# Optimization experiments

Hardware: AMD Instinct MI355X
Metric: run time of the kernel (lower is better)

Reference implementation:

```python
import jax, jax.numpy as jnp
import numpy as np

N, E, IN, HID, HEADS, OUT = 50000, 800000, 128, 64, 4, 64


def setup_inputs() -> dict:
    key = jax.random.key(0)
    ks = jax.random.split(key, 13)
    s1 = 1.0 / np.sqrt(IN)
    s2 = 1.0 / np.sqrt(HID * HEADS)
    s3 = 1.0 / np.sqrt(HID)
    return {
        'x': jax.random.normal(ks[0], (N, IN), dtype=jnp.float32),
        'edge_index': jax.random.randint(ks[1], (2, E), 0, N, dtype=jnp.int64),
        # GATv2 layer 1: heads=HEADS, out=HID, concat=True
        'W1l': jax.random.normal(ks[2], (IN, HEADS * HID), dtype=jnp.float32) * s1,
        'W1r': jax.random.normal(ks[3], (IN, HEADS * HID), dtype=jnp.float32) * s1,
        'att1': jax.random.normal(ks[4], (HEADS, HID), dtype=jnp.float32) * s3,
        'b1': jnp.zeros((HEADS * HID,), dtype=jnp.float32),
        # GATv2 layer 2: heads=1, out=HID
        'W2l': jax.random.normal(ks[5], (HEADS * HID, HID), dtype=jnp.float32) * s2,
        'W2r': jax.random.normal(ks[6], (HEADS * HID, HID), dtype=jnp.float32) * s2,
        'att2': jax.random.normal(ks[7], (1, HID), dtype=jnp.float32) * s3,
        'b2': jnp.zeros((HID,), dtype=jnp.float32),
        # final Linear(HID, OUT)
        'Wlin': jax.random.normal(ks[8], (HID, OUT), dtype=jnp.float32) * s3,
        'blin': jnp.zeros((OUT,), dtype=jnp.float32),
    }


def _gatv2(x, src, dst, Wl, Wr, att, bias, n):
    # PyG GATv2Conv (share_weights=False): x_j -> lin_l, x_i -> lin_r
    H, C = att.shape
    xl = (x @ Wl).reshape(n, H, C)  # source transform [N,H,C]
    xr = (x @ Wr).reshape(n, H, C)  # destination transform [N,H,C]
    # per-edge GATv2 score: a^T LeakyReLU(xl_j + xr_i)
    e = jnp.sum(jax.nn.leaky_relu(xl[src] + xr[dst], 0.2) * att, axis=-1)  # [E,H]
    # scatter-softmax over edges sharing a destination
    m = jax.ops.segment_max(e, dst, num_segments=n)  # [N,H]
    ex = jnp.exp(e - m[dst])
    denom = jax.ops.segment_sum(ex, dst, num_segments=n)
    alpha = ex / (denom[dst] + 1e-16)  # [E,H]
    # weighted scatter-add aggregation of source features
    out = jax.ops.segment_sum(xl[src] * alpha[:, :, None], dst, num_segments=n)  # [N,H,C]
    return out.reshape(n, H * C) + bias


def reference(x, edge_index, W1l, W1r, att1, b1, W2l, W2r, att2, b2, Wlin, blin):
    n = x.shape[0]
    loops = jnp.arange(n, dtype=edge_index.dtype)
    src = jnp.concatenate([edge_index[0], loops])  # add_self_loops=True (PyG default)
    dst = jnp.concatenate([edge_index[1], loops])
    h = _gatv2(x, src, dst, W1l, W1r, att1, b1, n)
    h = jax.nn.elu(h)
    h = _gatv2(h, src, dst, W2l, W2r, att2, b2, n)
    h = jax.nn.elu(h)
    return h @ Wlin + blin
```

## Files before the change

### kernel.cpp

```cpp
#include <hip/hip_runtime.h>
#include <hip/hip_bf16.h>
#include <math.h>

#define N_NODES 50000
#define N_EDGES 800000
#define ETOT (N_EDGES + N_NODES)
#define NB_SCAN 196

typedef __attribute__((ext_vector_type(8))) short short8;
typedef __attribute__((ext_vector_type(4))) float floatx4;
typedef __attribute__((ext_vector_type(2))) float f32x2;

__device__ __forceinline__ float bf_lo(unsigned u) { return __uint_as_float(u << 16); }
__device__ __forceinline__ float bf_hi(unsigned u) { return __uint_as_float(u & 0xffff0000u); }
__device__ __forceinline__ unsigned short f2bf(float f) {
    unsigned u = __float_as_uint(f);
    return (unsigned short)((u + 0x7fffu + ((u >> 16) & 1u)) >> 16);
}
__device__ __forceinline__ unsigned pack2bf(float a, float b) {
    return (unsigned)f2bf(a) | ((unsigned)f2bf(b) << 16);
}
#define DPP_ADD(p, ctrl) \
    (p) += __int_as_float(__builtin_amdgcn_update_dpp(0, __float_as_int(p), (ctrl), 0xF, 0xF, true))

__global__ __launch_bounds__(256) void k_prep(const float* __restrict__ W1l,
                                              const float* __restrict__ W1r,
                                              const float* __restrict__ W2l,
                                              const float* __restrict__ W2r,
                                              const float* __restrict__ Wlin,
                                              unsigned short* __restrict__ Wt1,
                                              unsigned short* __restrict__ Wt2,
                                              unsigned short* __restrict__ Wt3,
                                              int* __restrict__ deg) {
    const int b = blockIdx.x;
    if (b < 400) {
        const int idx = b * 256 + threadIdx.x;
        if (idx < 65536) {
            const int k = idx >> 9;
            const int n = idx & 511;
            const float v = (n < 256) ? W1l[k * 256 + n] : W1r[k * 256 + (n - 256)];
            Wt1[n * 128 + k] = f2bf(v);
        } else if (idx < 98304) {
            const int j = idx - 65536;
            const int k = j >> 7;
            const int n = j & 127;
            const float v = (n < 64) ? W2l[k * 64 + n] : W2r[k * 64 + (n - 64)];
            Wt2[n * 256 + k] = f2bf(v);
        } else {
            const int j = idx - 98304;
            const int n = j >> 6, k = j & 63;
            Wt3[n * 64 + k] = f2bf(Wlin[k * 64 + n]);
        }
    } else {
        const int i = (b - 400) * 256 + threadIdx.x;
        if (i < N_NODES) deg[i] = 0;
    }
}

__global__ __launch_bounds__(256) void k_g1h(const float* __restrict__ x,
                                             const unsigned short* __restrict__ Wt1,
                                             unsigned short* __restrict__ xlb,
                                             unsigned short* __restrict__ xrb,
                                             const int* __restrict__ ei,
                                             int* __restrict__ deg) {
    __shared__ unsigned short sA[128 * 136];
    const int b = blockIdx.x;
    if (b >= 782) {
        for (long e = (long)(b - 782) * 256 + threadIdx.x; e < ETOT; e += 1024 * 256) {
            const int d = (e < N_EDGES) ? ei[N_EDGES + e] : (int)(e - N_EDGES);
            atomicAdd(&deg[d], 1);
        }
        return;
    }
    const int t = threadIdx.x;
    const int lane = t & 63, wv = t >> 6;
    const int m0 = (b >> 1) * 128;
    const int flavor = b & 1;
#pragma unroll
    for (int j = 0; j < 16; j++) {
        const int i4 = t + j * 256;
        const int row = i4 >> 5, k4 = i4 & 31;
        float4 v = make_float4(0.f, 0.f, 0.f, 0.f);
        if (m0 + row < N_NODES) v = ((const float4*)x)[(long)(m0 + row) * 32 + k4];
        ushort4 u;
        u.x = f2bf(v.x); u.y = f2bf(v.y); u.z = f2bf(v.z); u.w = f2bf(v.w);
        *(ushort4*)&sA[row * 136 + k4 * 4] = u;
    }
    __syncthreads();
    const int l15 = lane & 15, quad = lane >> 4;
    const int nloc0 = wv * 64;
    unsigned short* outp = flavor ? xrb : xlb;
    short8 bfr[4][4];
#pragma unroll
    for (int nt = 0; nt < 4; nt++)
#pragma unroll
        for (int ks = 0; ks < 4; ks++)
            bfr[nt][ks] = *(const short8*)&Wt1[(flavor * 256 + nloc0 + nt * 16 + l15) * 128 + ks * 32 + quad * 8];
    for (int mt = 0; mt < 8; mt++) {
        short8 a[4];
#pragma unroll
        for (int ks = 0; ks < 4; ks++)
            a[ks] = *(const short8*)&sA[(mt * 16 + l15) * 136 + ks * 32 + quad * 8];
        floatx4 acc[4];
#pragma unroll
        for (int nt = 0; nt < 4; nt++) {
            acc[nt] = (floatx4)(0.f);
#pragma unroll
            for (int ks = 0; ks < 4; ks++)
                acc[nt] = __builtin_amdgcn_mfma_f32_16x16x32_bf16(a[ks], bfr[nt][ks], acc[nt], 0, 0, 0);
        }
        const int mrow0 = m0 + mt * 16 + quad * 4;
#pragma unroll
        for (int nt = 0; nt < 4; nt++) {
            const int n = nloc0 + nt * 16 + l15;
#pragma unroll
            for (int r = 0; r < 4; r++) {
                const int m = mrow0 + r;
                if (m < N_NODES) outp[(long)m * 256 + n] = f2bf(acc[nt][r]);
            }
        }
    }
}

__global__ __launch_bounds__(256) void k_scan1(const int* __restrict__ deg,
                                               int* __restrict__ rowstart,
                                               int* __restrict__ blocksum) {
    __shared__ int wsum[4];
    const int t = threadIdx.x, lane = t & 63, wv = t >> 6;
    const int i = blockIdx.x * 256 + t;
    const int v = (i < N_NODES) ? deg[i] : 0;
    int incl = v;
#pragma unroll
    for (int off = 1; off < 64; off <<= 1) {
        const int u = __shfl_up(incl, off);
        if (lane >= off) incl += u;
    }
    if (lane == 63) wsum[wv] = incl;
    __syncthreads();
    int woff = 0;
#pragma unroll
    for (int j = 0; j < 4; j++) woff += (j < wv) ? wsum[j] : 0;
    const int excl = incl - v + woff;
    if (i < N_NODES) rowstart[i] = excl;
    if (t == 255) blocksum[blockIdx.x] = excl + v;
}

__global__ __launch_bounds__(256) void k_scan2(const int* __restrict__ blocksum,
                                               int* __restrict__ blockoff) {
    __shared__ int wsum[4];
    const int t = threadIdx.x, lane = t & 63, wv = t >> 6;
    const int v = (t < NB_SCAN) ? blocksum[t] : 0;
    int incl = v;
#pragma unroll
    for (int off = 1; off < 64; off <<= 1) {
        const int u = __shfl_up(incl, off);
        if (lane >= off) incl += u;
    }
    if (lane == 63) wsum[wv] = incl;
    __syncthreads();
    int woff = 0;
#pragma unroll
    for (int j = 0; j < 4; j++) woff += (j < wv) ? wsum[j] : 0;
    if (t < NB_SCAN) blockoff[t] = incl - v + woff;
}

__global__ __launch_bounds__(256) void k_scan3(int* __restrict__ rowstart,
                                               const int* __restrict__ blockoff,
                                               int* __restrict__ cursor) {
    const int i = blockIdx.x * 256 + threadIdx.x;
    if (i < N_NODES) {
        const int r = rowstart[i] + blockoff[blockIdx.x];
        rowstart[i] = r;
        cursor[i] = r;
    }
}

__global__ __launch_bounds__(256) void k_scatter(const int* __restrict__ ei,
                                                 int* __restrict__ cursor,
                                                 int* __restrict__ csr) {
    const long e = (long)blockIdx.x * 256 + threadIdx.x;
    if (e >= ETOT) return;
    int s, d;
    if (e < N_EDGES) { s = ei[e]; d = ei[N_EDGES + e]; }
    else { s = d = (int)(e - N_EDGES); }
    const int pos = atomicAdd(&cursor[d], 1);
    csr[pos] = s << 9;
}

__global__ __launch_bounds__(256) void k_node1(const int* __restrict__ rowstart,
                                               const int* __restrict__ deg,
                                               const int* __restrict__ csr,
                                               const uint4* __restrict__ xlb,
                                               const uint4* __restrict__ xrb,
                                               const float* __restrict__ att,
                                               const float* __restrict__ b1,
                                               uint4* __restrict__ h1b) {
    const int lane = threadIdx.x & 63;
    const int wv = threadIdx.x >> 6;
    const int node = blockIdx.x * 4 + wv;
    const int g = lane >> 5;
    const int l = lane & 31;
    const char* xlbase = (const char*)xlb;
    const uint4 xru = xrb[(long)node * 32 + l];
    const float4 ta = ((const float4*)att)[2 * l];
    const float4 tb = ((const float4*)att)[2 * l + 1];
    f32x2 xp[4], tp[4];
    xp[0] = (f32x2){bf_lo(xru.x), bf_hi(xru.x)};
    xp[1] = (f32x2){bf_lo(xru.y), bf_hi(xru.y)};
    xp[2] = (f32x2){bf_lo(xru.z), bf_hi(xru.z)};
    xp[3] = (f32x2){bf_lo(xru.w), bf_hi(xru.w)};
    tp[0] = (f32x2){ta.x, ta.y}; tp[1] = (f32x2){ta.z, ta.w};
    tp[2] = (f32x2){tb.x, tb.y}; tp[3] = (f32x2){tb.z, tb.w};
    const int start = rowstart[node];
    const int cnt = deg[node];
    const int ns = (cnt - g + 1) >> 1;
    float den = 0.f;
    f32x2 acc[4];
#pragma unroll
    for (int c = 0; c < 4; c++) acc[c] = (f32x2)(0.f);

    auto body = [&](const uint4& rr) {
        f32x2 a0, a1, a2, a3;
        a0.x = bf_lo(rr.x); a0.y = bf_hi(rr.x);
        a1.x = bf_lo(rr.y); a1.y = bf_hi(rr.y);
        a2.x = bf_lo(rr.z); a2.y = bf_hi(rr.z);
        a3.x = bf_lo(rr.w); a3.y = bf_hi(rr.w);
        f32x2 v = a0 + xp[0];
        f32x2 p2 = __builtin_elementwise_max(v, v * 0.2f) * tp[0];
        v = a1 + xp[1]; p2 += __builtin_elementwise_max(v, v * 0.2f) * tp[1];
        v = a2 + xp[2]; p2 += __builtin_elementwise_max(v, v * 0.2f) * tp[2];
        v = a3 + xp[3]; p2 += __builtin_elementwise_max(v, v * 0.2f) * tp[3];
        float p = p2.x + p2.y;
        DPP_ADD(p, 0xB1);
        DPP_ADD(p, 0x4E);
        DPP_ADD(p, 0x141);
        const float w = __expf(p);
        acc[0] += a0 * w;
        acc[1] += a1 * w;
        acc[2] += a2 * w;
        acc[3] += a3 * w;
        den += w;
    };

    uint4 rcur = make_uint4(0, 0, 0, 0), rnext = rcur;
    if (ns > 0) rcur = *((const uint4*)(xlbase + csr[start + g]) + l);
    if (ns > 1) rnext = *((const uint4*)(xlbase + csr[start + 2 + g]) + l);
    int i = 0;
    for (; i + 2 < ns; i++) {
        const uint4 r2 = *((const uint4*)(xlbase + csr[start + 2 * (i + 2) + g]) + l);
        body(rcur);
        rcur = rnext; rnext = r2;
    }
    for (; i < ns; i++) {
        body(rcur);
        rcur = rnext;
    }
    den += __shfl_xor(den, 32);
    const float inv = 1.f / (den + 1e-16f);
#pragma unroll
    for (int c = 0; c < 4; c++) {
        f32x2 t2 = acc[c];
        t2.x += __shfl_xor(t2.x, 32);
        t2.y += __shfl_xor(t2.y, 32);
        acc[c] = t2;
    }
    const float4 ba = ((const float4*)b1)[2 * l];
    const float4 bb = ((const float4*)b1)[2 * l + 1];
    f32x2 bp[4];
    bp[0] = (f32x2){ba.x, ba.y}; bp[1] = (f32x2){ba.z, ba.w};
    bp[2] = (f32x2){bb.x, bb.y}; bp[3] = (f32x2){bb.z, bb.w};
    float o[8];
#pragma unroll
    for (int c = 0; c < 4; c++) {
        f32x2 t2 = acc[c] * inv + bp[c];
        o[2 * c]     = t2.x > 0.f ? t2.x : expm1f(t2.x);
        o[2 * c + 1] = t2.y > 0.f ? t2.y : expm1f(t2.y);
    }
    if (g == 0) {
        uint4 u;
        u.x = pack2bf(o[0], o[1]);
        u.y = pack2bf(o[2], o[3]);
        u.z = pack2bf(o[4], o[5]);
        u.w = pack2bf(o[6], o[7]);
        h1b[(long)node * 32 + l] = u;
    }
}

__global__ __launch_bounds__(256) void k_gemm2(const uint4* __restrict__ h,
                                               const unsigned short* __restrict__ Wt2,
                                               unsigned short* __restrict__ xlb,
                                               unsigned short* __restrict__ xrb) {
    __shared__ unsigned short sA[64 * 264];
    const int t = threadIdx.x;
    const int lane = t & 63, wv = t >> 6;
    const int m0 = blockIdx.x * 64;
#pragma unroll
    for (int j = 0; j < 8; j++) {
        const int i8 = t + j * 256;
        const int row = i8 >> 5, c8 = i8 & 31;
        uint4 v = make_uint4(0, 0, 0, 0);
        if (m0 + row < N_NODES) v = h[(long)(m0 + row) * 32 + c8];
        *(uint4*)&sA[row * 264 + c8 * 8] = v;
    }
    __syncthreads();
    const int l15 = lane & 15, quad = lane >> 4;
    const int ncol0 = wv * 32;
    short8 b[2][8];
#pragma unroll
    for (int nt = 0; nt < 2; nt++)
#pragma unroll
        for (int ks = 0; ks < 8; ks++)
            b[nt][ks] = *(const short8*)&Wt2[(ncol0 + nt * 16 + l15) * 256 + ks * 32 + quad * 8];
    for (int mt = 0; mt < 4; mt++) {
        floatx4 acc[2];
        acc[0] = (floatx4)(0.f);
        acc[1] = (floatx4)(0.f);
#pragma unroll
        for (int ks = 0; ks < 8; ks++) {
            const short8 a = *(const short8*)&sA[(mt * 16 + l15) * 264 + ks * 32 + quad * 8];
            acc[0] = __builtin_amdgcn_mfma_f32_16x16x32_bf16(a, b[0][ks], acc[0], 0, 0, 0);
            acc[1] = __builtin_amdgcn_mfma_f32_16x16x32_bf16(a, b[1][ks], acc[1], 0, 0, 0);
        }
        const int mrow0 = m0 + mt * 16 + quad * 4;
#pragma unroll
        for (int nt = 0; nt < 2; nt++) {
            const int n = ncol0 + nt * 16 + l15;
#pragma unroll
            for (int r = 0; r < 4; r++) {
                const int m = mrow0 + r;
                if (m < N_NODES) {
                    if (n < 64) xlb[(long)m * 64 + n] = f2bf(acc[nt][r]);
                    else        xrb[(long)m * 64 + (n - 64)] = f2bf(acc[nt][r]);
                }
            }
        }
    }
}

__global__ __launch_bounds__(256) void k_node2(const int* __restrict__ rowstart,
                                               const int* __restrict__ deg,
                                               const int* __restrict__ csr,
                                               const uint2* __restrict__ xlb,
                                               const uint2* __restrict__ xrb,
                                               const float* __restrict__ att,
                                               const float* __restrict__ b2,
                                               uint2* __restrict__ h2b) {
    const int lane = threadIdx.x & 63;
    const int wv = threadIdx.x >> 6;
    const int node = blockIdx.x * 4 + wv;
    const int g = lane >> 4;
    const int l = lane & 15;
    const char* xlbase = (const char*)xlb;
    const uint2 xru = xrb[(long)node * 16 + l];
    const float4 at4 = ((const float4*)att)[l];
    f32x2 xp[2], tp[2];
    xp[0] = (f32x2){bf_lo(xru.x), bf_hi(xru.x)};
    xp[1] = (f32x2){bf_lo(xru.y), bf_hi(xru.y)};
    tp[0] = (f32x2){at4.x, at4.y}; tp[1] = (f32x2){at4.z, at4.w};
    const int start = rowstart[node];
    const int cnt = deg[node];
    const int ns = (cnt - g + 3) >> 2;
    float den = 0.f;
    f32x2 acc[2];
    acc[0] = (f32x2)(0.f); acc[1] = (f32x2)(0.f);

    auto body = [&](const uint2& rr) {
        f32x2 a0, a1;
        a0.x = bf_lo(rr.x); a0.y = bf_hi(rr.x);
        a1.x = bf_lo(rr.y); a1.y = bf_hi(rr.y);
        f32x2 v = a0 + xp[0];
        f32x2 p2 = __builtin_elementwise_max(v, v * 0.2f) * tp[0];
        v = a1 + xp[1]; p2 += __builtin_elementwise_max(v, v * 0.2f) * tp[1];
        float p = p2.x + p2.y;
        DPP_ADD(p, 0xB1);
        DPP_ADD(p, 0x4E);
        DPP_ADD(p, 0x141);
        DPP_ADD(p, 0x140);
        const float w = __expf(p);
        acc[0] += a0 * w;
        acc[1] += a1 * w;
        den += w;
    };

    uint2 rcur = make_uint2(0, 0), rnext = rcur;
    if (ns > 0) rcur = *((const uint2*)(xlbase + (csr[start + g] >> 2)) + l);
    if (ns > 1) rnext = *((const uint2*)(xlbase + (csr[start + 4 + g] >> 2)) + l);
    int i = 0;
    for (; i + 2 < ns; i++) {
        const uint2 r2 = *((const uint2*)(xlbase + (csr[start + 4 * (i + 2) + g] >> 2)) + l);
        body(rcur);
        rcur = rnext; rnext = r2;
    }
    for (; i < ns; i++) {
        body(rcur);
        rcur = rnext;
    }
    den += __shfl_xor(den, 16);
    den += __shfl_xor(den, 32);
    const float inv = 1.f / (den + 1e-16f);
    float t0 = acc[0].x, t1 = acc[0].y, t2 = acc[1].x, t3 = acc[1].y;
    t0 += __shfl_xor(t0, 16); t0 += __shfl_xor(t0, 32);
    t1 += __shfl_xor(t1, 16); t1 += __shfl_xor(t1, 32);
    t2 += __shfl_xor(t2, 16); t2 += __shfl_xor(t2, 32);
    t3 += __shfl_xor(t3, 16); t3 += __shfl_xor(t3, 32);
    const float4 b4 = ((const float4*)b2)[l];
    float4 h4;
    h4.x = t0 * inv + b4.x; h4.x = h4.x > 0.f ? h4.x : expm1f(h4.x);
    h4.y = t1 * inv + b4.y; h4.y = h4.y > 0.f ? h4.y : expm1f(h4.y);
    h4.z = t2 * inv + b4.z; h4.z = h4.z > 0.f ? h4.z : expm1f(h4.z);
    h4.w = t3 * inv + b4.w; h4.w = h4.w > 0.f ? h4.w : expm1f(h4.w);
    if (g == 0) {
        uint2 u;
        u.x = pack2bf(h4.x, h4.y);
        u.y = pack2bf(h4.z, h4.w);
        h2b[(long)node * 16 + l] = u;
    }
}

__global__ __launch_bounds__(256) void k_gemm3(const uint4* __restrict__ h2,
                                               const unsigned short* __restrict__ Wt3,
                                               const float* __restrict__ blin,
                                               float* __restrict__ out) {
    __shared__ unsigned short sA[64 * 72];
    const int t = threadIdx.x;
    const int lane = t & 63, wv = t >> 6;
    const int m0 = blockIdx.x * 64;
#pragma unroll
    for (int j = 0; j < 2; j++) {
        const int i8 = t + j * 256;
        const int row = i8 >> 3, c8 = i8 & 7;
        uint4 v = make_uint4(0, 0, 0, 0);
        if (m0 + row < N_NODES) v = h2[(long)(m0 + row) * 8 + c8];
        *(uint4*)&sA[row * 72 + c8 * 8] = v;
    }
    __syncthreads();
    const int l15 = lane & 15, quad = lane >> 4;
    const int n0 = wv * 16;
    const short8 b0 = *(const short8*)&Wt3[(n0 + l15) * 64 + quad * 8];
    const short8 b1 = *(const short8*)&Wt3[(n0 + l15) * 64 + 32 + quad * 8];
    const float bl = blin[n0 + l15];
#pragma unroll
    for (int mt = 0; mt < 4; mt++) {
        const short8 a0 = *(const short8*)&sA[(mt * 16 + l15) * 72 + quad * 8];
        const short8 a1 = *(const short8*)&sA[(mt * 16 + l15) * 72 + 32 + quad * 8];
        floatx4 acc = (floatx4)(0.f);
        acc = __builtin_amdgcn_mfma_f32_16x16x32_bf16(a0, b0, acc, 0, 0, 0);
        acc = __builtin_amdgcn_mfma_f32_16x16x32_bf16(a1, b1, acc, 0, 0, 0);
        const int mrow0 = m0 + mt * 16 + quad * 4;
#pragma unroll
        for (int r = 0; r < 4; r++) {
            const int m = mrow0 + r;
            if (m < N_NODES) out[(long)m * 64 + n0 + l15] = acc[r] + bl;
        }
    }
}

extern "C" void kernel_launch(void* const* d_in, const int* in_sizes, int n_in,
                              void* d_out, int out_size, void* d_ws, size_t ws_size,
                              hipStream_t stream) {
    (void)in_sizes; (void)n_in; (void)out_size; (void)ws_size;
    const float* x    = (const float*)d_in[0];
    const int*   ei   = (const int*)d_in[1];
    const float* W1l  = (const float*)d_in[2];
    const float* W1r  = (const float*)d_in[3];
    const float* att1 = (const float*)d_in[4];
    const float* b1   = (const float*)d_in[5];
    const float* W2l  = (const float*)d_in[6];
    const float* W2r  = (const float*)d_in[7];
    const float* att2 = (const float*)d_in[8];
    const float* b2   = (const float*)d_in[9];
    const float* Wlin = (const float*)d_in[10];
    const float* blin = (const float*)d_in[11];

    float* ws = (float*)d_ws;
    unsigned short* XL1b = (unsigned short*)(ws);
    uint2*          H2b  = (uint2*)(ws);
    unsigned short* XR1b = (unsigned short*)(ws + 6400000);
    uint4*          H1b  = (uint4*)(ws + 12800000);
    unsigned short* XL2b = (unsigned short*)(ws + 19200000);
    unsigned short* XR2b = (unsigned short*)(ws + 20800000);
    int* deg      = (int*)(ws + 22400000);
    int* rowstart = deg + 50000;
    int* cursor   = rowstart + 50000;
    int* blocksum = cursor + 50000;
    int* blockoff = blocksum + 256;
    int* csr      = blockoff + 256;
    unsigned short* Wt1 = (unsigned short*)(ws + 23500000);
    unsigned short* Wt2 = (unsigned short*)(ws + 23550000);
    unsigned short* Wt3 = (unsigned short*)(ws + 23600000);

    k_prep<<<596, 256, 0, stream>>>(W1l, W1r, W2l, W2r, Wlin, Wt1, Wt2, Wt3, deg);
    k_g1h<<<1806, 256, 0, stream>>>(x, Wt1, XL1b, XR1b, ei, deg);
    k_scan1<<<NB_SCAN, 256, 0, stream>>>(deg, rowstart, blocksum);
    k_scan2<<<1, 256, 0, stream>>>(blocksum, blockoff);
    k_scan3<<<NB_SCAN, 256, 0, stream>>>(rowstart, blockoff, cursor);
    k_scatter<<<(ETOT + 255) / 256, 256, 0, stream>>>(ei, cursor, csr);
    k_node1<<<12500, 256, 0, stream>>>(rowstart, deg, csr,
                                       (const uint4*)XL1b, (const uint4*)XR1b,
                                       att1, b1, H1b);
    k_gemm2<<<782, 256, 0, stream>>>((const uint4*)H1b, Wt2, XL2b, XR2b);
    k_node2<<<12500, 256, 0, stream>>>(rowstart, deg, csr,
                                       (const uint2*)XL2b, (const uint2*)XR2b,
                                       att2, b2, H2b);
    k_gemm3<<<782, 256, 0, stream>>>((const uint4*)H2b, Wt3, blin, (float*)d_out);
}
```

Baseline: 314.9 us.

## Batch-load CSR indices per wave and deepen gather prefetch to four stages

In both GATv2 aggregation kernels, each wave now loads up to 64 CSR neighbor offsets with one coalesced load and broadcasts them via readlane. Previously every gather step issued its own dependent scalar index load. The gather loop keeps four outstanding feature loads instead of two, which raises memory-level parallelism. Tail edges are handled by clamping indices and masking their weights to zero, at the cost of some redundant loads and extra registers.

```diff
diff --git a/kernel.cpp b/kernel.cpp
--- a/kernel.cpp
+++ b/kernel.cpp
@@ -213,13 +213,12 @@
     tp[2] = (f32x2){tb.x, tb.y}; tp[3] = (f32x2){tb.z, tb.w};
     const int start = rowstart[node];
     const int cnt = deg[node];
-    const int ns = (cnt - g + 1) >> 1;
     float den = 0.f;
     f32x2 acc[4];
 #pragma unroll
     for (int c = 0; c < 4; c++) acc[c] = (f32x2)(0.f);
 
-    auto body = [&](const uint4& rr) {
+    auto body = [&](const uint4& rr, bool valid) {
         f32x2 a0, a1, a2, a3;
         a0.x = bf_lo(rr.x); a0.y = bf_hi(rr.x);
         a1.x = bf_lo(rr.y); a1.y = bf_hi(rr.y);
@@ -234,7 +233,8 @@
         DPP_ADD(p, 0xB1);
         DPP_ADD(p, 0x4E);
         DPP_ADD(p, 0x141);
-        const float w = __expf(p);
+        float w = __expf(p);
+        w = valid ? w : 0.f;
         acc[0] += a0 * w;
         acc[1] += a1 * w;
         acc[2] += a2 * w;
@@ -242,18 +242,34 @@
         den += w;
     };
 
-    uint4 rcur = make_uint4(0, 0, 0, 0), rnext = rcur;
-    if (ns > 0) rcur = *((const uint4*)(xlbase + csr[start + g]) + l);
-    if (ns > 1) rnext = *((const uint4*)(xlbase + csr[start + 2 + g]) + l);
-    int i = 0;
-    for (; i + 2 < ns; i++) {
-        const uint4 r2 = *((const uint4*)(xlbase + csr[start + 2 * (i + 2) + g]) + l);
-        body(rcur);
-        rcur = rnext; rnext = r2;
-    }
-    for (; i < ns; i++) {
-        body(rcur);
-        rcur = rnext;
+    for (int b0 = 0; b0 < cnt; b0 += 64) {
+        const int rem = min(64, cnt - b0);
+        const int it  = (rem + 1) >> 1;
+        const int last = it - 1;
+        const int idx = csr[start + b0 + (lane < rem ? lane : rem - 1)];
+        auto off_at = [&](int j) {
+            const int jj = j < last ? j : last;
+            const int e0 = __builtin_amdgcn_readlane(idx, 2 * jj);
+            const int e1 = __builtin_amdgcn_readlane(idx, 2 * jj + 1);
+            return g ? e1 : e0;
+        };
+        auto ld = [&](int off) { return *((const uint4*)(xlbase + off) + l); };
+
+        uint4 r0 = ld(off_at(0));
+        uint4 r1 = ld(off_at(1));
+        uint4 r2 = ld(off_at(2));
+        uint4 r3 = ld(off_at(3));
+        int i = 0;
+        for (; i + 4 < it; i += 4) {
+            uint4 n0 = ld(off_at(i + 4)); body(r0, true); r0 = n0;
+            uint4 n1 = ld(off_at(i + 5)); body(r1, true); r1 = n1;
+            uint4 n2 = ld(off_at(i + 6)); body(r2, true); r2 = n2;
+            uint4 n3 = ld(off_at(i + 7)); body(r3, true); r3 = n3;
+        }
+        body(r0, (2 * i + g) < rem);
+        if (i + 1 < it) body(r1, (2 * (i + 1) + g) < rem);
+        if (i + 2 < it) body(r2, (2 * (i + 2) + g) < rem);
+        if (i + 3 < it) body(r3, (2 * (i + 3) + g) < rem);
     }
     den += __shfl_xor(den, 32);
     const float inv = 1.f / (den + 1e-16f);
@@ -359,12 +375,11 @@
     tp[0] = (f32x2){at4.x, at4.y}; tp[1] = (f32x2){at4.z, at4.w};
     const int start = rowstart[node];
     const int cnt = deg[node];
-    const int ns = (cnt - g + 3) >> 2;
     float den = 0.f;
     f32x2 acc[2];
     acc[0] = (f32x2)(0.f); acc[1] = (f32x2)(0.f);
 
-    auto body = [&](const uint2& rr) {
+    auto body = [&](const uint2& rr, bool valid) {
         f32x2 a0, a1;
         a0.x = bf_lo(rr.x); a0.y = bf_hi(rr.x);
         a1.x = bf_lo(rr.y); a1.y = bf_hi(rr.y);
@@ -376,24 +391,45 @@
         DPP_ADD(p, 0x4E);
         DPP_ADD(p, 0x141);
         DPP_ADD(p, 0x140);
-        const float w = __expf(p);
+        float w = __expf(p);
+        w = valid ? w : 0.f;
         acc[0] += a0 * w;
         acc[1] += a1 * w;
         den += w;
     };
 
-    uint2 rcur = make_uint2(0, 0), rnext = rcur;
-    if (ns > 0) rcur = *((const uint2*)(xlbase + (csr[start + g] >> 2)) + l);
-    if (ns > 1) rnext = *((const uint2*)(xlbase + (csr[start + 4 + g] >> 2)) + l);
-    int i = 0;
-    for (; i + 2 < ns; i++) {
-        const uint2 r2 = *((const uint2*)(xlbase + (csr[start + 4 * (i + 2) + g] >> 2)) + l);
-        body(rcur);
-        rcur = rnext; rnext = r2;
-    }
-    for (; i < ns; i++) {
-        body(rcur);
-        rcur = rnext;
+    for (int b0 = 0; b0 < cnt; b0 += 64) {
+        const int rem = min(64, cnt - b0);
+        const int it  = (rem + 3) >> 2;
+        const int last = it - 1;
+        const int idx = csr[start + b0 + (lane < rem ? lane : rem - 1)];
+        auto off_at = [&](int j) {
+            const int jj = j < last ? j : last;
+            const int e0 = __builtin_amdgcn_readlane(idx, 4 * jj);
+            const int e1 = __builtin_amdgcn_readlane(idx, 4 * jj + 1);
+            const int e2 = __builtin_amdgcn_readlane(idx, 4 * jj + 2);
+            const int e3 = __builtin_amdgcn_readlane(idx, 4 * jj + 3);
+            const int elo = (g & 1) ? e1 : e0;
+            const int ehi = (g & 1) ? e3 : e2;
+            return ((g & 2) ? ehi : elo) >> 2;
+        };
+        auto ld = [&](int off) { return *((const uint2*)(xlbase + off) + l); };
+
+        uint2 r0 = ld(off_at(0));
+        uint2 r1 = ld(off_at(1));
+        uint2 r2 = ld(off_at(2));
+        uint2 r3 = ld(off_at(3));
+        int i = 0;
+        for (; i + 4 < it; i += 4) {
+            uint2 n0 = ld(off_at(i + 4)); body(r0, true); r0 = n0;
+            uint2 n1 = ld(off_at(i + 5)); body(r1, true); r1 = n1;
+            uint2 n2 = ld(off_at(i + 6)); body(r2, true); r2 = n2;
+            uint2 n3 = ld(off_at(i + 7)); body(r3, true); r3 = n3;
+        }
+        body(r0, (4 * i + g) < rem);
+        if (i + 1 < it) body(r1, (4 * (i + 1) + g) < rem);
+        if (i + 2 < it) body(r2, (4 * (i + 2) + g) < rem);
+        if (i + 3 < it) body(r3, (4 * (i + 3) + g) < rem);
     }
     den += __shfl_xor(den, 16);
     den += __shfl_xor(den, 32);
```

After: 329.5 us. 1.05x slower.

## Fuse final linear into layer-2 node kernel and merge GEMM1 flavors per block

Applied to the files above, without the earlier changes.

The final Linear(HID,OUT) is folded into k_node2. Each wave writes its fp32 ELU output to shared memory and then computes a 64x64 matvec with the fp32 Wlin weights. This removes the k_gemm3 launch and the bf16 H2 round trip through global memory, but replaces MFMA with scalar FMAs and per-lane global weight reads. Separately, k_g1h now computes both the left and right projections inside one block, so the x tile is loaded and converted to bf16 once instead of twice. The cost is half as many GEMM blocks, each doing twice the work.

```diff
diff --git a/kernel.cpp b/kernel.cpp
--- a/kernel.cpp
+++ b/kernel.cpp
@@ -65,8 +65,8 @@
                                              int* __restrict__ deg) {
     __shared__ unsigned short sA[128 * 136];
     const int b = blockIdx.x;
-    if (b >= 782) {
-        for (long e = (long)(b - 782) * 256 + threadIdx.x; e < ETOT; e += 1024 * 256) {
+    if (b >= 391) {
+        for (long e = (long)(b - 391) * 256 + threadIdx.x; e < ETOT; e += 1024 * 256) {
             const int d = (e < N_EDGES) ? ei[N_EDGES + e] : (int)(e - N_EDGES);
             atomicAdd(&deg[d], 1);
         }
@@ -74,8 +74,7 @@
     }
     const int t = threadIdx.x;
     const int lane = t & 63, wv = t >> 6;
-    const int m0 = (b >> 1) * 128;
-    const int flavor = b & 1;
+    const int m0 = b * 128;
 #pragma unroll
     for (int j = 0; j < 16; j++) {
         const int i4 = t + j * 256;
@@ -89,34 +88,36 @@
     __syncthreads();
     const int l15 = lane & 15, quad = lane >> 4;
     const int nloc0 = wv * 64;
-    unsigned short* outp = flavor ? xrb : xlb;
-    short8 bfr[4][4];
-#pragma unroll
-    for (int nt = 0; nt < 4; nt++)
-#pragma unroll
-        for (int ks = 0; ks < 4; ks++)
-            bfr[nt][ks] = *(const short8*)&Wt1[(flavor * 256 + nloc0 + nt * 16 + l15) * 128 + ks * 32 + quad * 8];
-    for (int mt = 0; mt < 8; mt++) {
-        short8 a[4];
-#pragma unroll
-        for (int ks = 0; ks < 4; ks++)
-            a[ks] = *(const short8*)&sA[(mt * 16 + l15) * 136 + ks * 32 + quad * 8];
-        floatx4 acc[4];
-#pragma unroll
-        for (int nt = 0; nt < 4; nt++) {
-            acc[nt] = (floatx4)(0.f);
+    for (int flavor = 0; flavor < 2; ++flavor) {
+        unsigned short* outp = flavor ? xrb : xlb;
+        short8 bfr[4][4];
+#pragma unroll
+        for (int nt = 0; nt < 4; nt++)
 #pragma unroll
             for (int ks = 0; ks < 4; ks++)
-                acc[nt] = __builtin_amdgcn_mfma_f32_16x16x32_bf16(a[ks], bfr[nt][ks], acc[nt], 0, 0, 0);
-        }
-        const int mrow0 = m0 + mt * 16 + quad * 4;
-#pragma unroll
-        for (int nt = 0; nt < 4; nt++) {
-            const int n = nloc0 + nt * 16 + l15;
-#pragma unroll
-            for (int r = 0; r < 4; r++) {
-                const int m = mrow0 + r;
-                if (m < N_NODES) outp[(long)m * 256 + n] = f2bf(acc[nt][r]);
+                bfr[nt][ks] = *(const short8*)&Wt1[(flavor * 256 + nloc0 + nt * 16 + l15) * 128 + ks * 32 + quad * 8];
+        for (int mt = 0; mt < 8; mt++) {
+            short8 a[4];
+#pragma unroll
+            for (int ks = 0; ks < 4; ks++)
+                a[ks] = *(const short8*)&sA[(mt * 16 + l15) * 136 + ks * 32 + quad * 8];
+            floatx4 acc[4];
+#pragma unroll
+            for (int nt = 0; nt < 4; nt++) {
+                acc[nt] = (floatx4)(0.f);
+#pragma unroll
+                for (int ks = 0; ks < 4; ks++)
+                    acc[nt] = __builtin_amdgcn_mfma_f32_16x16x32_bf16(a[ks], bfr[nt][ks], acc[nt], 0, 0, 0);
+            }
+            const int mrow0 = m0 + mt * 16 + quad * 4;
+#pragma unroll
+            for (int nt = 0; nt < 4; nt++) {
+                const int n = nloc0 + nt * 16 + l15;
+#pragma unroll
+                for (int r = 0; r < 4; r++) {
+                    const int m = mrow0 + r;
+                    if (m < N_NODES) outp[(long)m * 256 + n] = f2bf(acc[nt][r]);
+                }
             }
         }
     }
@@ -344,7 +345,10 @@
                                                const uint2* __restrict__ xrb,
                                                const float* __restrict__ att,
                                                const float* __restrict__ b2,
-                                               uint2* __restrict__ h2b) {
+                                               const float* __restrict__ Wlin,
+                                               const float* __restrict__ blin,
+                                               float* __restrict__ out) {
+    __shared__ float sh[4][64];
     const int lane = threadIdx.x & 63;
     const int wv = threadIdx.x >> 6;
     const int node = blockIdx.x * 4 + wv;
@@ -410,49 +414,17 @@
     h4.z = t2 * inv + b4.z; h4.z = h4.z > 0.f ? h4.z : expm1f(h4.z);
     h4.w = t3 * inv + b4.w; h4.w = h4.w > 0.f ? h4.w : expm1f(h4.w);
     if (g == 0) {
-        uint2 u;
-        u.x = pack2bf(h4.x, h4.y);
-        u.y = pack2bf(h4.z, h4.w);
-        h2b[(long)node * 16 + l] = u;
-    }
-}
-
-__global__ __launch_bounds__(256) void k_gemm3(const uint4* __restrict__ h2,
-                                               const unsigned short* __restrict__ Wt3,
-                                               const float* __restrict__ blin,
-                                               float* __restrict__ out) {
-    __shared__ unsigned short sA[64 * 72];
-    const int t = threadIdx.x;
-    const int lane = t & 63, wv = t >> 6;
-    const int m0 = blockIdx.x * 64;
-#pragma unroll
-    for (int j = 0; j < 2; j++) {
-        const int i8 = t + j * 256;
-        const int row = i8 >> 3, c8 = i8 & 7;
-        uint4 v = make_uint4(0, 0, 0, 0);
-        if (m0 + row < N_NODES) v = h2[(long)(m0 + row) * 8 + c8];
-        *(uint4*)&sA[row * 72 + c8 * 8] = v;
+        sh[wv][4 * l + 0] = h4.x;
+        sh[wv][4 * l + 1] = h4.y;
+        sh[wv][4 * l + 2] = h4.z;
+        sh[wv][4 * l + 3] = h4.w;
     }
     __syncthreads();
-    const int l15 = lane & 15, quad = lane >> 4;
-    const int n0 = wv * 16;
-    const short8 b0 = *(const short8*)&Wt3[(n0 + l15) * 64 + quad * 8];
-    const short8 b1 = *(const short8*)&Wt3[(n0 + l15) * 64 + 32 + quad * 8];
-    const float bl = blin[n0 + l15];
-#pragma unroll
-    for (int mt = 0; mt < 4; mt++) {
-        const short8 a0 = *(const short8*)&sA[(mt * 16 + l15) * 72 + quad * 8];
-        const short8 a1 = *(const short8*)&sA[(mt * 16 + l15) * 72 + 32 + quad * 8];
-        floatx4 acc = (floatx4)(0.f);
-        acc = __builtin_amdgcn_mfma_f32_16x16x32_bf16(a0, b0, acc, 0, 0, 0);
-        acc = __builtin_amdgcn_mfma_f32_16x16x32_bf16(a1, b1, acc, 0, 0, 0);
-        const int mrow0 = m0 + mt * 16 + quad * 4;
-#pragma unroll
-        for (int r = 0; r < 4; r++) {
-            const int m = mrow0 + r;
-            if (m < N_NODES) out[(long)m * 64 + n0 + l15] = acc[r] + bl;
-        }
-    }
+    float s = blin[lane];
+#pragma unroll
+    for (int k = 0; k < 64; k++)
+        s += sh[wv][k] * Wlin[k * 64 + lane];
+    out[(long)node * 64 + lane] = s;
 }
 
 extern "C" void kernel_launch(void* const* d_in, const int* in_sizes, int n_in,
@@ -474,7 +446,6 @@
 
     float* ws = (float*)d_ws;
     unsigned short* XL1b = (unsigned short*)(ws);
-    uint2*          H2b  = (uint2*)(ws);
     unsigned short* XR1b = (unsigned short*)(ws + 6400000);
     uint4*          H1b  = (uint4*)(ws + 12800000);
     unsigned short* XL2b = (unsigned short*)(ws + 19200000);
@@ -490,7 +461,7 @@
     unsigned short* Wt3 = (unsigned short*)(ws + 23600000);
 
     k_prep<<<596, 256, 0, stream>>>(W1l, W1r, W2l, W2r, Wlin, Wt1, Wt2, Wt3, deg);
-    k_g1h<<<1806, 256, 0, stream>>>(x, Wt1, XL1b, XR1b, ei, deg);
+    k_g1h<<<1415, 256, 0, stream>>>(x, Wt1, XL1b, XR1b, ei, deg);
     k_scan1<<<NB_SCAN, 256, 0, stream>>>(deg, rowstart, blocksum);
     k_scan2<<<1, 256, 0, stream>>>(blocksum, blockoff);
     k_scan3<<<NB_SCAN, 256, 0, stream>>>(rowstart, blockoff, cursor);
@@ -501,6 +472,5 @@
     k_gemm2<<<782, 256, 0, stream>>>((const uint4*)H1b, Wt2, XL2b, XR2b);
     k_node2<<<12500, 256, 0, stream>>>(rowstart, deg, csr,
                                        (const uint2*)XL2b, (const uint2*)XR2b,
-                                       att2, b2, H2b);
-    k_gemm3<<<782, 256, 0, stream>>>((const uint4*)H2b, Wt3, blin, (float*)d_out);
-}
+                                       att2, b2, Wlin, blin, (float*)d_out);
+}
```

After: 333.3 us. 5.9% more time.

## Build CSR via two-level bucket sort instead of global atomic degree count

Applied to the files above, without the earlier changes.

Replaces the per-node global atomic degree count, three-kernel scan and atomic scatter with a two-level bucket sort. Edges are first histogrammed by destination group of 256 in shared memory and scanned once. They are then scattered into coarse buckets through padded per-group cursors, and each bucket is finely sorted in shared memory to produce rowstart, deg and the CSR. The layer-1 GEMM blocks now compute both the left and right projections per block, halving the GEMM block count. This cuts kernel launches and contention on global atomics, at the cost of an extra pass over edges, a single-block scan that reads the whole partial-count table, and high contention on only 196 coarse cursors.

```diff
diff --git a/kernel.cpp b/kernel.cpp
--- a/kernel.cpp
+++ b/kernel.cpp
@@ -5,7 +5,8 @@
 #define N_NODES 50000
 #define N_EDGES 800000
 #define ETOT (N_EDGES + N_NODES)
-#define NB_SCAN 196
+#define NGRP 196
+#define HBLK 416
 
 typedef __attribute__((ext_vector_type(8))) short short8;
 typedef __attribute__((ext_vector_type(4))) float floatx4;
@@ -31,10 +32,13 @@
                                               unsigned short* __restrict__ Wt1,
                                               unsigned short* __restrict__ Wt2,
                                               unsigned short* __restrict__ Wt3,
-                                              int* __restrict__ deg) {
+                                              const int* __restrict__ ei,
+                                              unsigned* __restrict__ part) {
+    __shared__ unsigned sh[256];
     const int b = blockIdx.x;
+    const int t = threadIdx.x;
     if (b < 400) {
-        const int idx = b * 256 + threadIdx.x;
+        const int idx = b * 256 + t;
         if (idx < 65536) {
             const int k = idx >> 9;
             const int n = idx & 511;
@@ -51,10 +55,45 @@
             const int n = j >> 6, k = j & 63;
             Wt3[n * 64 + k] = f2bf(Wlin[k * 64 + n]);
         }
-    } else {
-        const int i = (b - 400) * 256 + threadIdx.x;
-        if (i < N_NODES) deg[i] = 0;
-    }
+        return;
+    }
+    const int bb = b - 400;
+    sh[t] = 0;
+    __syncthreads();
+#pragma unroll
+    for (int j = 0; j < 8; j++) {
+        const int e = bb * 2048 + j * 256 + t;
+        if (e < ETOT) {
+            const int d = (e < N_EDGES) ? ei[N_EDGES + e] : (e - N_EDGES);
+            atomicAdd(&sh[d >> 8], 1u);
+        }
+    }
+    __syncthreads();
+    part[bb * 256 + t] = sh[t];
+}
+
+__global__ __launch_bounds__(256) void k_scang(const unsigned* __restrict__ part,
+                                               int* __restrict__ g_off,
+                                               unsigned* __restrict__ cursor1pad) {
+    __shared__ int wsum[4];
+    const int t = threadIdx.x, lane = t & 63, wv = t >> 6;
+    unsigned s = 0;
+    for (int bb = 0; bb < HBLK; bb++) s += part[bb * 256 + t];
+    const int v = (int)s;
+    int incl = v;
+#pragma unroll
+    for (int off = 1; off < 64; off <<= 1) {
+        const int u = __shfl_up(incl, off);
+        if (lane >= off) incl += u;
+    }
+    if (lane == 63) wsum[wv] = incl;
+    __syncthreads();
+    int woff = 0;
+#pragma unroll
+    for (int j = 0; j < 4; j++) woff += (j < wv) ? wsum[j] : 0;
+    const int excl = incl - v + woff;
+    g_off[t] = excl;
+    cursor1pad[t * 16] = (unsigned)excl;
 }
 
 __global__ __launch_bounds__(256) void k_g1h(const float* __restrict__ x,
@@ -62,20 +101,29 @@
                                              unsigned short* __restrict__ xlb,
                                              unsigned short* __restrict__ xrb,
                                              const int* __restrict__ ei,
-                                             int* __restrict__ deg) {
+                                             unsigned* __restrict__ cursor1pad,
+                                             unsigned* __restrict__ tmp) {
     __shared__ unsigned short sA[128 * 136];
     const int b = blockIdx.x;
-    if (b >= 782) {
-        for (long e = (long)(b - 782) * 256 + threadIdx.x; e < ETOT; e += 1024 * 256) {
-            const int d = (e < N_EDGES) ? ei[N_EDGES + e] : (int)(e - N_EDGES);
-            atomicAdd(&deg[d], 1);
+    const int t = threadIdx.x;
+    if (b >= 391) {
+        const int bb = b - 391;
+#pragma unroll
+        for (int j = 0; j < 8; j++) {
+            const int e = bb * 2048 + j * 256 + t;
+            if (e < ETOT) {
+                int s, d;
+                if (e < N_EDGES) { s = ei[e]; d = ei[N_EDGES + e]; }
+                else { s = d = e - N_EDGES; }
+                const unsigned item = ((unsigned)d << 16) | (unsigned)s;
+                const unsigned pos = atomicAdd(&cursor1pad[(d >> 8) * 16], 1u);
+                tmp[pos] = item;
+            }
         }
         return;
     }
-    const int t = threadIdx.x;
     const int lane = t & 63, wv = t >> 6;
-    const int m0 = (b >> 1) * 128;
-    const int flavor = b & 1;
+    const int m0 = b * 128;
 #pragma unroll
     for (int j = 0; j < 16; j++) {
         const int i4 = t + j * 256;
@@ -89,46 +137,59 @@
     __syncthreads();
     const int l15 = lane & 15, quad = lane >> 4;
     const int nloc0 = wv * 64;
-    unsigned short* outp = flavor ? xrb : xlb;
-    short8 bfr[4][4];
-#pragma unroll
-    for (int nt = 0; nt < 4; nt++)
-#pragma unroll
-        for (int ks = 0; ks < 4; ks++)
-            bfr[nt][ks] = *(const short8*)&Wt1[(flavor * 256 + nloc0 + nt * 16 + l15) * 128 + ks * 32 + quad * 8];
-    for (int mt = 0; mt < 8; mt++) {
-        short8 a[4];
-#pragma unroll
-        for (int ks = 0; ks < 4; ks++)
-            a[ks] = *(const short8*)&sA[(mt * 16 + l15) * 136 + ks * 32 + quad * 8];
-        floatx4 acc[4];
-#pragma unroll
-        for (int nt = 0; nt < 4; nt++) {
-            acc[nt] = (floatx4)(0.f);
+    for (int flavor = 0; flavor < 2; ++flavor) {
+        unsigned short* outp = flavor ? xrb : xlb;
+        short8 bfr[4][4];
+#pragma unroll
+        for (int nt = 0; nt < 4; nt++)
 #pragma unroll
             for (int ks = 0; ks < 4; ks++)
-                acc[nt] = __builtin_amdgcn_mfma_f32_16x16x32_bf16(a[ks], bfr[nt][ks], acc[nt], 0, 0, 0);
-        }
-        const int mrow0 = m0 + mt * 16 + quad * 4;
-#pragma unroll
-        for (int nt = 0; nt < 4; nt++) {
-            const int n = nloc0 + nt * 16 + l15;
-#pragma unroll
-            for (int r = 0; r < 4; r++) {
-                const int m = mrow0 + r;
-                if (m < N_NODES) outp[(long)m * 256 + n] = f2bf(acc[nt][r]);
+                bfr[nt][ks] = *(const short8*)&Wt1[(flavor * 256 + nloc0 + nt * 16 + l15) * 128 + ks * 32 + quad * 8];
+        for (int mt = 0; mt < 8; mt++) {
+            short8 a[4];
+#pragma unroll
+            for (int ks = 0; ks < 4; ks++)
+                a[ks] = *(const short8*)&sA[(mt * 16 + l15) * 136 + ks * 32 + quad * 8];
+            floatx4 acc[4];
+#pragma unroll
+            for (int nt = 0; nt < 4; nt++) {
+                acc[nt] = (floatx4)(0.f);
+#pragma unroll
+                for (int ks = 0; ks < 4; ks++)
+                    acc[nt] = __builtin_amdgcn_mfma_f32_16x16x32_bf16(a[ks], bfr[nt][ks], acc[nt], 0, 0, 0);
             }
-        }
-    }
-}
-
-__global__ __launch_bounds__(256) void k_scan1(const int* __restrict__ deg,
+            const int mrow0 = m0 + mt * 16 + quad * 4;
+#pragma unroll
+            for (int nt = 0; nt < 4; nt++) {
+                const int n = nloc0 + nt * 16 + l15;
+#pragma unroll
+                for (int r = 0; r < 4; r++) {
+                    const int m = mrow0 + r;
+                    if (m < N_NODES) outp[(long)m * 256 + n] = f2bf(acc[nt][r]);
+                }
+            }
+        }
+    }
+}
+
+__global__ __launch_bounds__(256) void k_bsort(const unsigned* __restrict__ tmp,
+                                               const int* __restrict__ g_off,
                                                int* __restrict__ rowstart,
-                                               int* __restrict__ blocksum) {
+                                               int* __restrict__ deg,
+                                               int* __restrict__ csr) {
+    __shared__ unsigned h[256];
+    __shared__ unsigned cur[256];
     __shared__ int wsum[4];
     const int t = threadIdx.x, lane = t & 63, wv = t >> 6;
-    const int i = blockIdx.x * 256 + t;
-    const int v = (i < N_NODES) ? deg[i] : 0;
+    const int g = blockIdx.x;
+    const int base = g_off[g];
+    const int n = g_off[g + 1] - base;
+    h[t] = 0;
+    __syncthreads();
+    for (int i = t; i < n; i += 256)
+        atomicAdd(&h[(tmp[base + i] >> 16) & 255u], 1u);
+    __syncthreads();
+    const int v = (int)h[t];
     int incl = v;
 #pragma unroll
     for (int off = 1; off < 64; off <<= 1) {
@@ -141,50 +202,18 @@
 #pragma unroll
     for (int j = 0; j < 4; j++) woff += (j < wv) ? wsum[j] : 0;
     const int excl = incl - v + woff;
-    if (i < N_NODES) rowstart[i] = excl;
-    if (t == 255) blocksum[blockIdx.x] = excl + v;
-}
-
-__global__ __launch_bounds__(256) void k_scan2(const int* __restrict__ blocksum,
-                                               int* __restrict__ blockoff) {
-    __shared__ int wsum[4];
-    const int t = threadIdx.x, lane = t & 63, wv = t >> 6;
-    const int v = (t < NB_SCAN) ? blocksum[t] : 0;
-    int incl = v;
-#pragma unroll
-    for (int off = 1; off < 64; off <<= 1) {
-        const int u = __shfl_up(incl, off);
-        if (lane >= off) incl += u;
-    }
-    if (lane == 63) wsum[wv] = incl;
-    __syncthreads();
-    int woff = 0;
-#pragma unroll
-    for (int j = 0; j < 4; j++) woff += (j < wv) ? wsum[j] : 0;
-    if (t < NB_SCAN) blockoff[t] = incl - v + woff;
-}
-
-__global__ __launch_bounds__(256) void k_scan3(int* __restrict__ rowstart,
-                                               const int* __restrict__ blockoff,
-                                               int* __restrict__ cursor) {
-    const int i = blockIdx.x * 256 + threadIdx.x;
-    if (i < N_NODES) {
-        const int r = rowstart[i] + blockoff[blockIdx.x];
-        rowstart[i] = r;
-        cursor[i] = r;
-    }
-}
-
-__global__ __launch_bounds__(256) void k_scatter(const int* __restrict__ ei,
-                                                 int* __restrict__ cursor,
-                                                 int* __restrict__ csr) {
-    const long e = (long)blockIdx.x * 256 + threadIdx.x;
-    if (e >= ETOT) return;
-    int s, d;
-    if (e < N_EDGES) { s = ei[e]; d = ei[N_EDGES + e]; }
-    else { s = d = (int)(e - N_EDGES); }
-    const int pos = atomicAdd(&cursor[d], 1);
-    csr[pos] = s << 9;
+    const int d = g * 256 + t;
+    if (d < N_NODES) {
+        rowstart[d] = base + excl;
+        deg[d] = v;
+    }
+    cur[t] = (unsigned)excl;
+    __syncthreads();
+    for (int i = t; i < n; i += 256) {
+        const unsigned item = tmp[base + i];
+        const unsigned p = atomicAdd(&cur[(item >> 16) & 255u], 1u);
+        csr[base + (int)p] = (int)((item & 0xFFFFu) << 9);
+    }
 }
 
 __global__ __launch_bounds__(256) void k_node1(const int* __restrict__ rowstart,
@@ -477,24 +506,24 @@
     uint2*          H2b  = (uint2*)(ws);
     unsigned short* XR1b = (unsigned short*)(ws + 6400000);
     uint4*          H1b  = (uint4*)(ws + 12800000);
+    unsigned*       part = (unsigned*)(ws + 12800000);
+    unsigned*       tmp  = (unsigned*)(ws + 12800000);
     unsigned short* XL2b = (unsigned short*)(ws + 19200000);
     unsigned short* XR2b = (unsigned short*)(ws + 20800000);
-    int* deg      = (int*)(ws + 22400000);
-    int* rowstart = deg + 50000;
-    int* cursor   = rowstart + 50000;
-    int* blocksum = cursor + 50000;
-    int* blockoff = blocksum + 256;
-    int* csr      = blockoff + 256;
+    int* deg       = (int*)(ws + 22400000);
+    int* rowstart  = (int*)(ws + 22450000);
+    int* csr       = (int*)(ws + 22550000);
+    unsigned* cursor1pad = (unsigned*)(ws + 23420000);
+    int*      g_off      = (int*)(ws + 23430000);
     unsigned short* Wt1 = (unsigned short*)(ws + 23500000);
     unsigned short* Wt2 = (unsigned short*)(ws + 23550000);
     unsigned short* Wt3 = (unsigned short*)(ws + 23600000);
 
-    k_prep<<<596, 256, 0, stream>>>(W1l, W1r, W2l, W2r, Wlin, Wt1, Wt2, Wt3, deg);
-    k_g1h<<<1806, 256, 0, stream>>>(x, Wt1, XL1b, XR1b, ei, deg);
-    k_scan1<<<NB_SCAN, 256, 0, stream>>>(deg, rowstart, blocksum);
-    k_scan2<<<1, 256, 0, stream>>>(blocksum, blockoff);
-    k_scan3<<<NB_SCAN, 256, 0, stream>>>(rowstart, blockoff, cursor);
-    k_scatter<<<(ETOT + 255) / 256, 256, 0, stream>>>(ei, cursor, csr);
+    k_prep<<<400 + HBLK, 256, 0, stream>>>(W1l, W1r, W2l, W2r, Wlin,
+                                           Wt1, Wt2, Wt3, ei, part);
+    k_scang<<<1, 256, 0, stream>>>(part, g_off, cursor1pad);
+    k_g1h<<<391 + HBLK, 256, 0, stream>>>(x, Wt1, XL1b, XR1b, ei, cursor1pad, tmp);
+    k_bsort<<<NGRP, 256, 0, stream>>>(tmp, g_off, rowstart, deg, csr);
     k_node1<<<12500, 256, 0, stream>>>(rowstart, deg, csr,
                                        (const uint4*)XL1b, (const uint4*)XR1b,
                                        att1, b1, H1b);
```

Result: slower. 351.1 us (+11.5%).
